# Performance work log

Measured on AMD Instinct MI355X. Metric: run time of the kernel, lower is better.

## Reference

```python
import jax, jax.numpy as jnp
import numpy as np
import math

INPUT_SIZE = 4096
PTS_PER_EPOCH = 100


def _grid_bounds(input_size):
    # Replicates get_grid(): n_row = n_col = ceil(sqrt(input_size)),
    # each cell is the central half of its grid square (gap = size/4 on each side).
    n = math.ceil(math.sqrt(input_size))
    size = 1.0 / n
    gap = size / 4.0
    i = jnp.arange(input_size)
    gy = i // n  # row index (uses n_row == n_col)
    gx = i % n
    x_low = gx.astype(jnp.float32) * size + gap
    y_low = gy.astype(jnp.float32) * size + gap
    x_high = x_low + 2.0 * gap
    y_high = y_low + 2.0 * gap
    return x_low, x_high, y_low, y_high


def setup_inputs() -> dict:
    key = jax.random.key(0)
    k1, k2, k3 = jax.random.split(key, 3)
    batch = 8192
    n_fibers = 64
    total_pts = 10000  # 100 * max_epoch
    inp = jax.random.normal(k1, (batch, INPUT_SIZE), dtype=jnp.float32)
    fibers_x = jax.random.uniform(k2, (n_fibers, total_pts), dtype=jnp.float32)
    fibers_y = jax.random.uniform(k3, (n_fibers, total_pts), dtype=jnp.float32)
    return {"input": inp, "fibers_x": fibers_x, "fibers_y": fibers_y, "current_epoch": 7}


def reference(input, fibers_x, fibers_y, current_epoch):
    t = current_epoch * PTS_PER_EPOCH
    # points of all fibers for this epoch, flattened: (P,) with P = n_fibers*100
    px = fibers_x[:, t:t + PTS_PER_EPOCH].reshape(-1)
    py = fibers_y[:, t:t + PTS_PER_EPOCH].reshape(-1)
    x_low, x_high, y_low, y_high = _grid_bounds(INPUT_SIZE)
    # broadcast point-in-rectangle test: (P, 1) vs (N,) -> (P, N)
    in_cell = ((x_low[None, :] <= px[:, None]) & (px[:, None] <= x_high[None, :]) &
               (y_low[None, :] <= py[:, None]) & (py[:, None] <= y_high[None, :]))
    touching = jnp.any(in_cell, axis=0)  # (N,)
    mask = jnp.where(touching, 0.0, 1.0).astype(input.dtype)
    return input * mask[None, :]
```

## Files before the change

### kernel.cpp

```cpp
#include <hip/hip_runtime.h>


#define N_COLS 4096
#define PTS_PER_EPOCH 100
#define N_GRID 64
#define TOTAL_PTS 10000
#define N_FIBERS 64
#define BLOCK 256
#define GRID_BLOCKS 2048
#define CHUNK4 4096

typedef float f32x4 __attribute__((ext_vector_type(4)));

__global__ __launch_bounds__(BLOCK) void fused_fbm_dropout(
    const float* __restrict__ fx,
    const float* __restrict__ fy,
    const int* __restrict__ epoch_p,
    const f32x4* __restrict__ in4,
    f32x4* __restrict__ out4,
    int n4) {
    __shared__ float mask[N_COLS];
    const int tid = threadIdx.x;

    for (int i = tid; i < N_COLS; i += BLOCK) mask[i] = 1.0f;
    __syncthreads();

    const int t = epoch_p[0] * PTS_PER_EPOCH;
    for (int g = tid; g < (N_FIBERS * PTS_PER_EPOCH) / 4; g += BLOCK) {
        const int f  = g / 25;
        const int j4 = g - f * 25;
        const int base4 = (f * TOTAL_PTS + t) / 4 + j4;
        const f32x4 px4 = ((const f32x4*)fx)[base4];
        const f32x4 py4 = ((const f32x4*)fy)[base4];
#pragma unroll
        for (int k = 0; k < 4; ++k) {
            const float ux = px4[k] * 64.0f;
            const float uy = py4[k] * 64.0f;
            const float gxf = floorf(ux);
            const float gyf = floorf(uy);
            const float frx = ux - gxf;
            const float fry = uy - gyf;
            if (frx >= 0.25f && frx <= 0.75f && fry >= 0.25f && fry <= 0.75f) {
                const int gx = (int)gxf;
                const int gy = (int)gyf;
                if (gx >= 0 && gx < N_GRID && gy >= 0 && gy < N_GRID) {
                    mask[gy * N_GRID + gx] = 0.0f;
                }
            }
        }
    }
    __syncthreads();

    const int base = blockIdx.x * CHUNK4;
    f32x4 m[4];
#pragma unroll
    for (int k = 0; k < 4; ++k)
        m[k] = ((const f32x4*)mask)[(k * BLOCK + tid) & (N_COLS / 4 - 1)];

    if (base + CHUNK4 <= n4) {
#pragma unroll
        for (int r = 0; r < 4; ++r) {
            f32x4 a[4];
#pragma unroll
            for (int c = 0; c < 4; ++c)
                a[c] = in4[base + (r * 4 + c) * BLOCK + tid];
#pragma unroll
            for (int c = 0; c < 4; ++c) {
                const f32x4 v = a[c] * m[c];
                __builtin_nontemporal_store(v, &out4[base + (r * 4 + c) * BLOCK + tid]);
            }
        }
    } else {
        for (int k = 0; k < CHUNK4 / BLOCK; ++k) {
            const int i = base + k * BLOCK + tid;
            if (i < n4) {
                const f32x4 v = in4[i] * m[k & 3];
                __builtin_nontemporal_store(v, &out4[i]);
            }
        }
    }
}

extern "C" void kernel_launch(void* const* d_in, const int* in_sizes, int n_in,
                              void* d_out, int out_size, void* d_ws, size_t ws_size,
                              hipStream_t stream) {
    const float* inp   = (const float*)d_in[0];
    const float* fx    = (const float*)d_in[1];
    const float* fy    = (const float*)d_in[2];
    const int*   epoch = (const int*)d_in[3];

    const int n4 = out_size / 4;
    fused_fbm_dropout<<<GRID_BLOCKS, BLOCK, 0, stream>>>(
        fx, fy, epoch, (const f32x4*)inp, (f32x4*)d_out, n4);
}
```

Measured before the change: 250.8 us.

## Prefetch input before mask build and switch to grid-stride streaming

```diff
diff --git a/kernel.cpp b/kernel.cpp
--- a/kernel.cpp
+++ b/kernel.cpp
@@ -8,7 +8,9 @@
 #define N_FIBERS 64
 #define BLOCK 256
 #define GRID_BLOCKS 2048
-#define CHUNK4 4096
+#define STRIDE (GRID_BLOCKS * BLOCK)
+#define ITER 16
+#define PF 8
 
 typedef float f32x4 __attribute__((ext_vector_type(4)));
 
@@ -21,6 +23,14 @@
     int n4) {
     __shared__ float mask[N_COLS];
     const int tid = threadIdx.x;
+    const int i0 = blockIdx.x * BLOCK + tid;
+    const bool fast = (n4 == GRID_BLOCKS * BLOCK * ITER);
+
+    f32x4 a[PF];
+    if (fast) {
+#pragma unroll
+        for (int k = 0; k < PF; ++k) a[k] = in4[i0 + k * STRIDE];
+    }
 
     for (int i = tid; i < N_COLS; i += BLOCK) mask[i] = 1.0f;
     __syncthreads();
@@ -51,32 +61,19 @@
     }
     __syncthreads();
 
-    const int base = blockIdx.x * CHUNK4;
-    f32x4 m[4];
+    const f32x4 m = ((const f32x4*)mask)[i0 & (N_COLS / 4 - 1)];
+
+    if (fast) {
 #pragma unroll
-    for (int k = 0; k < 4; ++k)
-        m[k] = ((const f32x4*)mask)[(k * BLOCK + tid) & (N_COLS / 4 - 1)];
-
-    if (base + CHUNK4 <= n4) {
-#pragma unroll
-        for (int r = 0; r < 4; ++r) {
-            f32x4 a[4];
-#pragma unroll
-            for (int c = 0; c < 4; ++c)
-                a[c] = in4[base + (r * 4 + c) * BLOCK + tid];
-#pragma unroll
-            for (int c = 0; c < 4; ++c) {
-                const f32x4 v = a[c] * m[c];
-                __builtin_nontemporal_store(v, &out4[base + (r * 4 + c) * BLOCK + tid]);
-            }
+        for (int k = 0; k < ITER; ++k) {
+            const f32x4 v = a[k & (PF - 1)] * m;
+            if (k + PF < ITER)
+                a[k & (PF - 1)] = in4[i0 + (k + PF) * STRIDE];
+            out4[i0 + k * STRIDE] = v;
         }
     } else {
-        for (int k = 0; k < CHUNK4 / BLOCK; ++k) {
-            const int i = base + k * BLOCK + tid;
-            if (i < n4) {
-                const f32x4 v = in4[i] * m[k & 3];
-                __builtin_nontemporal_store(v, &out4[i]);
-            }
+        for (int i = i0; i < n4; i += STRIDE) {
+            out4[i] = in4[i] * m;
         }
     }
 }
```

After: 249.2 us. Within noise of the previous version (-0.7%).
